# Optimization experiments

Measured on AMD Instinct MI355X. Metric: run time of the kernel, lower is better.

The kernel has to match this reference:

```python
import jax, jax.numpy as jnp
import numpy as np

B, T, L, IN, D, H = 2, 16, 256, 768, 1024, 16
HD = D // H
NREG = 4
P = NREG + 2          # frozen prefix: registers + noise + action
DEPTH = 8
TINT = 4              # temporal_attention_interval
CTX = 30              # temporal_context_length
BASE = 1000.0         # rope_base
EPS = 1e-6            # qk_norm_eps / rmsnorm eps
HID = 4096            # 4.0 * latent_dim
S = L + P             # tokens per frame


def _rms(x, w=None, eps=EPS):
    y = x * jax.lax.rsqrt(jnp.mean(x * x, axis=-1, keepdims=True) + eps)
    return y * w if w is not None else y


def _rope_cache(n, hd, base):
    inv = base ** (-jnp.arange(0, hd, 2, dtype=jnp.float32) / hd)
    ang = jnp.arange(n, dtype=jnp.float32)[:, None] * inv[None, :]  # [n, hd/2]
    return jnp.cos(ang), jnp.sin(ang)


def _apply_rope(x, cos, sin):
    x1, x2 = x[..., ::2], x[..., 1::2]
    return jnp.stack([x1 * cos - x2 * sin, x1 * sin + x2 * cos], axis=-1).reshape(x.shape)


def _attn(x, Wqkv, Wo, cos, sin, mask):
    # x: [..., S, D]; mask: bool, True = attend, broadcastable to [..., H, S, S]
    qkv = x @ Wqkv
    q, k, v = jnp.split(qkv, 3, axis=-1)
    heads = lambda t: t.reshape(t.shape[:-1] + (H, HD)).swapaxes(-2, -3)  # [..., H, S, HD]
    q, k, v = heads(q), heads(k), heads(v)
    q = _apply_rope(_rms(q), cos, sin)   # qk-norm then RoPE
    k = _apply_rope(_rms(k), cos, sin)
    s = jnp.einsum('...qd,...kd->...qk', q, k) / jnp.sqrt(jnp.float32(HD))
    s = jnp.where(mask, s, jnp.float32(-1e9))
    p = jax.nn.softmax(s, axis=-1) * mask.any(axis=-1, keepdims=True)  # zero rows with no allowed keys
    o = jnp.einsum('...qk,...kd->...qd', p, v)
    return o.swapaxes(-2, -3).reshape(x.shape) @ Wo


def _spatial_mask():
    m = np.zeros((S, S), bool)
    r, n, a, ls = NREG, NREG, NREG + 1, NREG + 2
    m[ls:, ls:] = True; m[ls:, n] = True; m[ls:, a] = True; m[ls:, :r] = True
    m[n, n] = True; m[a, a] = True
    m[:r, ls:] = True; m[:r, n] = True; m[:r, a] = True; m[:r, :r] = True
    return jnp.asarray(m)


def _temporal_mask(indep):
    m = jnp.tril(jnp.ones((T, T), bool), -1)  # strictly-past causal
    if CTX is not None and CTX < T:
        m = m & jnp.triu(m, -CTX)             # sliding context window
    m = jnp.broadcast_to(m, (B, T, T))
    m = jnp.where(indep[:, None, None], False, m)
    return m[:, None, None]  # [B,1,1,T,T] -> broadcasts over token pos and heads


def setup_inputs() -> dict:
    key = jax.random.key(0)
    ks = iter(jax.random.split(key, 40))
    g = lambda shape, s=0.02: jax.random.normal(next(ks), shape, jnp.float32) * s
    inp = {
        'noisy_latents': jax.random.normal(next(ks), (B, T, L, IN), jnp.float32),
        'noise_levels': jax.random.uniform(next(ks), (B, T), jnp.float32),
        'actions': jax.random.normal(next(ks), (B, T, 6), jnp.float32),
        'independent_frames_mask': jnp.zeros((B,), bool),
        'actions_mask': jnp.ones((B, T), bool),
        'W_in': g((IN, D)),
        'noise_w1': g((1, D)), 'noise_b1': jnp.zeros((D,), jnp.float32),
        'noise_w2': g((D, D)), 'noise_b2': jnp.zeros((D,), jnp.float32),
        'base_action_embed': g((D,)),
        'action_w': g((6, D)), 'action_b': jnp.zeros((D,), jnp.float32),
        'registers': g((NREG, D)),
        'ln1_w': jnp.ones((DEPTH, D), jnp.float32),
        'Wqkv_s': g((DEPTH, D, 3 * D)), 'Wo_s': g((DEPTH, D, D)),
        'lnt_w': jnp.ones((DEPTH, D), jnp.float32),
        'Wqkv_t': g((DEPTH, D, 3 * D)), 'Wo_t': g((DEPTH, D, D)),
        'ln2_w': jnp.ones((DEPTH, D), jnp.float32),
        'W1': g((DEPTH, D, HID)), 'W2': g((DEPTH, D, HID)), 'W3': g((DEPTH, HID, D)),
        'final_w': jnp.ones((D,), jnp.float32),
        'W_out': g((D, IN)), 'b_out': jnp.zeros((IN,), jnp.float32),
    }
    return inp


def reference(noisy_latents, noise_levels, actions, independent_frames_mask, actions_mask,
              W_in, noise_w1, noise_b1, noise_w2, noise_b2, base_action_embed,
              action_w, action_b, registers, ln1_w, Wqkv_s, Wo_s, lnt_w, Wqkv_t, Wo_t,
              ln2_w, W1, W2, W3, final_w, W_out, b_out):
    noisy_tokens = noisy_latents @ W_in                                   # [B,T,L,D]
    base = jnp.broadcast_to(base_action_embed, (B, T, 1, D))
    act = base + (actions @ action_w + action_b)[:, :, None, :]
    act = jnp.where(actions_mask[:, :, None, None], act, base)            # [B,T,1,D]
    nz = jax.nn.silu(noise_levels[..., None] @ noise_w1 + noise_b1) @ noise_w2 + noise_b2
    nz = nz[:, :, None, :]                                                # [B,T,1,D]
    reg = jnp.broadcast_to(registers, (B, T, NREG, D))
    x = jnp.concatenate([reg, nz, act, noisy_tokens], axis=2)             # [B,T,S,D]

    sp_mask = _spatial_mask()
    tm_mask = _temporal_mask(independent_frames_mask)
    sp_cos, sp_sin = _rope_cache(S, HD, BASE)
    tm_cos, tm_sin = _rope_cache(T, HD, BASE)
    keep_tok = (jnp.arange(S) >= P)[None, :, None, None]                  # zero temporal update on frozen prefix

    for i in range(DEPTH):
        h = _rms(x, ln1_w[i])
        x = x + _attn(h, Wqkv_s[i], Wo_s[i], sp_cos, sp_sin, sp_mask)
        if i % TINT == 0:
            ht = _rms(x, lnt_w[i]).transpose(0, 2, 1, 3)                  # [B,S,T,D]
            ot = _attn(ht, Wqkv_t[i], Wo_t[i], tm_cos, tm_sin, tm_mask)
            x = x + (ot * keep_tok).transpose(0, 2, 1, 3)
        h2 = _rms(x, ln2_w[i])
        x = x + (jax.nn.silu(h2 @ W1[i]) * (h2 @ W2[i])) @ W3[i]

    latents = _rms(x[..., P:, :], final_w)
    pred_clean_latents = latents @ W_out + b_out                          # [B,T,L,IN]
    return pred_clean_latents
```

## Files before the change

kernel.cpp:

```cpp
#include <hip/hip_runtime.h>
#include <cstdint>
#include <cstddef>

#define DEV __device__ __forceinline__

typedef __attribute__((ext_vector_type(8))) __bf16 bf16x8;
typedef __attribute__((ext_vector_type(4))) float f32x4;

#define NTOK   8384
#define NTOKP  8448
#define NLAT   8192

DEV float b2f(unsigned short u) {
  unsigned int x = ((unsigned int)u) << 16;
  return __builtin_bit_cast(float, x);
}
DEV unsigned short f2b(float f) {
  unsigned int x = __builtin_bit_cast(unsigned int, f);
  x += 0x7fffu + ((x >> 16) & 1u);
  return (unsigned short)(x >> 16);
}
DEV float wred_sum(float v) {
#pragma unroll
  for (int o = 32; o; o >>= 1) v += __shfl_xor(v, o);
  return v;
}
DEV bool mask_or(const void* p, int i) {
  return ((const unsigned char*)p)[i] != 0 || ((const int*)p)[i] != 0;
}
DEV bool mask_and(const void* p, int i) {
  return ((const unsigned char*)p)[i] != 0 && ((const int*)p)[i] != 0;
}


__global__ void conv_f2b(const float* __restrict__ in, unsigned short* __restrict__ out, int n4) {
  int i = blockIdx.x * 256 + threadIdx.x;
  if (i < n4) {
    float4 v = ((const float4*)in)[i];
    ushort4 o;
    o.x = f2b(v.x); o.y = f2b(v.y); o.z = f2b(v.z); o.w = f2b(v.w);
    ((ushort4*)out)[i] = o;
  }
}

__global__ void build_rope(float2* __restrict__ out, int npos) {
  int idx = blockIdx.x * 256 + threadIdx.x;
  if (idx >= npos * 32) return;
  int pos = idx >> 5, i = idx & 31;
  float inv = powf(1000.0f, -(float)(2 * i) * (1.0f / 64.0f));
  float ang = (float)pos * inv;
  float sv, cv;
  sincosf(ang, &sv, &cv);
  out[idx] = make_float2(cv, sv);
}

__global__ __launch_bounds__(256) void transpose_w(const float* __restrict__ in,
                                                   unsigned short* __restrict__ out,
                                                   int K, int N, int ostride, int mode) {
  __shared__ float tile[32][33];
  int kb = blockIdx.x * 32, nb = blockIdx.y * 32;
  int tx = threadIdx.x & 31, ty = threadIdx.x >> 5;
#pragma unroll
  for (int i = 0; i < 32; i += 8)
    tile[ty + i][tx] = in[(size_t)(kb + ty + i) * N + (nb + tx)];
  __syncthreads();
#pragma unroll
  for (int i = 0; i < 32; i += 8) {
    int n = nb + ty + i;
    int row = n;
    if (mode == 1) row = ((n >> 4) << 5) | (n & 15);
    else if (mode == 2) row = (((n >> 4) << 5) + 16) | (n & 15);
    out[(size_t)row * ostride + (kb + tx)] = f2b(tile[tx][ty + i]);
  }
}

__global__ __launch_bounds__(256) void noise_h1(const float* __restrict__ nlvl,
                                                const float* __restrict__ w1,
                                                const float* __restrict__ b1,
                                                const float* __restrict__ b2,
                                                float* __restrict__ h1,
                                                float* __restrict__ nz) {
  int i = blockIdx.x * 256 + threadIdx.x;
  int bt = i >> 10, d = i & 1023;
  float v = nlvl[bt] * w1[d] + b1[d];
  h1[i] = v / (1.0f + expf(-v));
  nz[i] = b2[d];
}

__global__ __launch_bounds__(256) void noise_mm(const float* __restrict__ h1,
                                                const float* __restrict__ w2,
                                                float* __restrict__ nz) {
  __shared__ float hs[32][128];
  int kc = blockIdx.x >> 4, dpg = blockIdx.x & 15;
  int tid = threadIdx.x;
  int k0 = kc * 128;
  for (int idx = tid; idx < 32 * 128; idx += 256) {
    int bt = idx >> 7, k = idx & 127;
    hs[bt][k] = h1[bt * 1024 + k0 + k];
  }
  __syncthreads();
  int dp = dpg * 64 + (tid & 63);
  int bt0 = (tid >> 6) * 8;
  float acc[8] = {};
  for (int k = 0; k < 128; ++k) {
    float w = w2[(size_t)(k0 + k) * 1024 + dp];
#pragma unroll
    for (int j = 0; j < 8; ++j) acc[j] += hs[bt0 + j][k] * w;
  }
#pragma unroll
  for (int j = 0; j < 8; ++j) atomicAdd(&nz[(bt0 + j) * 1024 + dp], acc[j]);
}

__global__ void embed_special(float* __restrict__ x, const float* __restrict__ regs,
                              const float* __restrict__ nz, const float* __restrict__ base_emb,
                              const float* __restrict__ actions, const float* __restrict__ action_w,
                              const float* __restrict__ action_b,
                              const void* __restrict__ amask) {
  int bt = blockIdx.x, d = threadIdx.x;
  float* xr = x + (size_t)bt * 262 * 1024;
#pragma unroll
  for (int r = 0; r < 4; ++r) xr[r * 1024 + d] = regs[r * 1024 + d];
  xr[4 * 1024 + d] = nz[(size_t)bt * 1024 + d];
  float a = base_emb[d];
  if (mask_or(amask, bt)) {
    float s = action_b[d];
#pragma unroll
    for (int i = 0; i < 6; ++i) s += actions[bt * 6 + i] * action_w[i * 1024 + d];
    a += s;
  }
  xr[5 * 1024 + d] = a;
}

template <bool REMAP>
__global__ __launch_bounds__(256) void rms_k(const float* __restrict__ x,
                                             const float* __restrict__ w,
                                             unsigned short* __restrict__ out) {
  int m = blockIdx.x, tid = threadIdx.x;
  size_t src = REMAP ? ((size_t)(m >> 8) * 262 + 6 + (m & 255)) : (size_t)m;
  float4 v = ((const float4*)(x + src * 1024))[tid];
  float ss = v.x * v.x + v.y * v.y + v.z * v.z + v.w * v.w;
  ss = wred_sum(ss);
  __shared__ float sred[4];
  if ((tid & 63) == 0) sred[tid >> 6] = ss;
  __syncthreads();
  float tot = sred[0] + sred[1] + sred[2] + sred[3];
  float sc = rsqrtf(tot * (1.0f / 1024.0f) + 1e-6f);
  float4 wv = ((const float4*)w)[tid];
  ushort4 o;
  o.x = f2b(v.x * sc * wv.x); o.y = f2b(v.y * sc * wv.y);
  o.z = f2b(v.z * sc * wv.z); o.w = f2b(v.w * sc * wv.w);
  ((ushort4*)(out + (size_t)m * 1024))[tid] = o;
}

#define KSTR 72
#define VSTR 296
__global__ __launch_bounds__(256) void attn_spatial(const unsigned short* __restrict__ qkv,
                                                    unsigned short* __restrict__ o,
                                                    const float2* __restrict__ rope) {
  __shared__ unsigned short Ks[272 * KSTR];
  __shared__ unsigned short Vt[64 * VSTR];
  __shared__ unsigned short Ps[4][16 * VSTR];
  const int h = blockIdx.x & 15;
  const int bt = blockIdx.x >> 4;
  const int tid = threadIdx.x, wave = tid >> 6, lane = tid & 63;
  const size_t tb = (size_t)bt * 262;

  {
    const int d = lane;
#pragma unroll 1
    for (int pss = 0; pss < 17; ++pss) {
      const int t0 = (pss * 4 + wave) * 4;
      ushort4 vp;
      unsigned short* vpp = (unsigned short*)&vp;
#pragma unroll
      for (int j = 0; j < 4; ++j) {
        const int t = t0 + j;
        float kv = 0.f, vv = 0.f;
        if (t < 262) {
          const size_t rb = (tb + t) * 3072 + h * 64 + d;
          kv = b2f(qkv[rb + 1024]);
          vv = b2f(qkv[rb + 2048]);
        }
        float ss = wred_sum(kv * kv);
        kv *= rsqrtf(ss * (1.0f / 64.0f) + 1e-6f);
        float partner = __shfl_xor(kv, 1);
        const int tc = t < 262 ? t : 261;
        float2 cs = rope[tc * 32 + (d >> 1)];
        kv = ((d & 1) == 0) ? (kv * cs.x - partner * cs.y)
                            : (partner * cs.y + kv * cs.x);
        Ks[t * KSTR + d] = f2b(kv);
        vpp[j] = f2b(vv);
      }
      *(ushort4*)(&Vt[d * VSTR + t0]) = vp;
    }
    for (int idx = tid; idx < 64 * 24; idx += 256) {
      Vt[(idx / 24) * VSTR + 272 + (idx % 24)] = 0;
    }
    for (int idx = tid; idx < 4 * 16 * 34; idx += 256) {
      int w = idx / (16 * 34), r = (idx / 34) & 15, c = idx % 34;
      Ps[w][r * VSTR + 262 + c] = 0;
    }
  }
  __syncthreads();

  unsigned short* Pw = &Ps[wave][0];
  const int kcol = lane & 15;
  const int g8 = (lane >> 4) << 3;
  const int g4 = g8 >> 1;
  const int rq = (lane >> 4) << 2;

#pragma unroll 1
  for (int qc = wave; qc < 17; qc += 4) {
    const int q0 = qc * 16;
    const int qrow = q0 + kcol;
    const int grow = qrow < 262 ? qrow : 261;
    const unsigned short* qp = qkv + (tb + grow) * 3072 + h * 64 + g8;
    float qv[16];
    {
      ushort4 a = *(const ushort4*)qp, b = *(const ushort4*)(qp + 4);
      ushort4 c = *(const ushort4*)(qp + 32), e = *(const ushort4*)(qp + 36);
      qv[0] = b2f(a.x); qv[1] = b2f(a.y); qv[2] = b2f(a.z); qv[3] = b2f(a.w);
      qv[4] = b2f(b.x); qv[5] = b2f(b.y); qv[6] = b2f(b.z); qv[7] = b2f(b.w);
      qv[8] = b2f(c.x); qv[9] = b2f(c.y); qv[10] = b2f(c.z); qv[11] = b2f(c.w);
      qv[12] = b2f(e.x); qv[13] = b2f(e.y); qv[14] = b2f(e.z); qv[15] = b2f(e.w);
    }
    float ss = 0.f;
#pragma unroll
    for (int i = 0; i < 16; ++i) ss += qv[i] * qv[i];
    ss += __shfl_xor(ss, 16);
    ss += __shfl_xor(ss, 32);
    const float qsc = rsqrtf(ss * (1.0f / 64.0f) + 1e-6f);
    bf16x8 aq0, aq1;
    unsigned short* u0 = (unsigned short*)&aq0;
    unsigned short* u1 = (unsigned short*)&aq1;
#pragma unroll
    for (int i = 0; i < 4; ++i) {
      float2 cs0 = rope[grow * 32 + g4 + i];
      float a = qv[2 * i] * qsc, b = qv[2 * i + 1] * qsc;
      u0[2 * i] = f2b(a * cs0.x - b * cs0.y);
      u0[2 * i + 1] = f2b(a * cs0.y + b * cs0.x);
      float2 cs1 = rope[grow * 32 + 16 + g4 + i];
      float a1 = qv[8 + 2 * i] * qsc, b1 = qv[9 + 2 * i] * qsc;
      u1[2 * i] = f2b(a1 * cs1.x - b1 * cs1.y);
      u1[2 * i + 1] = f2b(a1 * cs1.y + b1 * cs1.x);
    }
    f32x4 sc[17];
#pragma unroll
    for (int kc = 0; kc < 17; ++kc) {
      const unsigned short* kb = &Ks[(kc * 16 + kcol) * KSTR + g8];
      f32x4 z = {};
      z = __builtin_amdgcn_mfma_f32_16x16x32_bf16(aq0, *(const bf16x8*)kb, z, 0, 0, 0);
      sc[kc] = __builtin_amdgcn_mfma_f32_16x16x32_bf16(aq1, *(const bf16x8*)(kb + 32), z, 0, 0, 0);
    }
#pragma unroll
    for (int kc = 0; kc < 17; ++kc) {
      const int k = kc * 16 + kcol;
#pragma unroll
      for (int j = 0; j < 4; ++j) {
        const int sq = q0 + rq + j;
        const bool valid = (k < 262) && ((sq != 4 && sq != 5) || (k == sq));
        sc[kc][j] = valid ? sc[kc][j] * 0.125f : -1e30f;
      }
    }
    float sm[4];
#pragma unroll
    for (int j = 0; j < 4; ++j) {
      float m = -1e30f;
#pragma unroll
      for (int kc = 0; kc < 17; ++kc) m = fmaxf(m, sc[kc][j]);
#pragma unroll
      for (int off = 1; off < 16; off <<= 1) m = fmaxf(m, __shfl_xor(m, off));
      float s = 0.f;
#pragma unroll
      for (int kc = 0; kc < 17; ++kc) {
        float e = expf(sc[kc][j] - m);
        sc[kc][j] = e;
        s += e;
      }
#pragma unroll
      for (int off = 1; off < 16; off <<= 1) s += __shfl_xor(s, off);
      sm[j] = 1.0f / s;
    }
#pragma unroll
    for (int kc = 0; kc < 17; ++kc) {
      const int k = kc * 16 + kcol;
#pragma unroll
      for (int j = 0; j < 4; ++j)
        Pw[(rq + j) * VSTR + k] = f2b(sc[kc][j] * sm[j]);
    }
    f32x4 oacc[4] = {};
#pragma unroll
    for (int tc = 0; tc < 9; ++tc) {
      const bf16x8 ap = *(const bf16x8*)(&Pw[kcol * VSTR + tc * 32 + g8]);
#pragma unroll
      for (int nt = 0; nt < 4; ++nt) {
        const bf16x8 bv = *(const bf16x8*)(&Vt[(nt * 16 + kcol) * VSTR + tc * 32 + g8]);
        oacc[nt] = __builtin_amdgcn_mfma_f32_16x16x32_bf16(ap, bv, oacc[nt], 0, 0, 0);
      }
    }
#pragma unroll
    for (int nt = 0; nt < 4; ++nt) {
#pragma unroll
      for (int j = 0; j < 4; ++j) {
        const int sq = q0 + rq + j;
        if (sq < 262)
          o[(tb + sq) * 1024 + h * 64 + nt * 16 + kcol] = f2b(oacc[nt][j]);
      }
    }
  }
}

__global__ __launch_bounds__(256) void attn_temporal(const unsigned short* __restrict__ qkv,
                                                     unsigned short* __restrict__ o,
                                                     const float2* __restrict__ rope,
                                                     const void* __restrict__ indep) {
  int gw = blockIdx.x * 4 + (threadIdx.x >> 6);
  int lane = threadIdx.x & 63;
  if (gw >= NTOK) return;
  int h = gw & 15;
  int s = (gw >> 4) % 262;
  int b = (gw >> 4) / 262;
  bool dead = (s < 6) || mask_and(indep, b);
  float q[16], kk[16], vv[16], out[16];
#pragma unroll
  for (int t = 0; t < 16; ++t) {
    out[t] = 0.f;
    if (!dead) {
      size_t off = ((size_t)((b * 16 + t) * 262 + s)) * 3072 + h * 64 + lane;
      q[t] = b2f(qkv[off]);
      kk[t] = b2f(qkv[off + 1024]);
      vv[t] = b2f(qkv[off + 2048]);
    }
  }
  if (!dead) {
#pragma unroll
    for (int t = 0; t < 16; ++t) {
      float sq_ = wred_sum(q[t] * q[t]);
      float qv = q[t] * rsqrtf(sq_ * (1.0f / 64.0f) + 1e-6f);
      float sk_ = wred_sum(kk[t] * kk[t]);
      float kv = kk[t] * rsqrtf(sk_ * (1.0f / 64.0f) + 1e-6f);
      float2 cs = rope[t * 32 + (lane >> 1)];
      float qp = __shfl_xor(qv, 1);
      float kp = __shfl_xor(kv, 1);
      q[t] = ((lane & 1) == 0) ? (qv * cs.x - qp * cs.y) : (qp * cs.y + qv * cs.x);
      kk[t] = ((lane & 1) == 0) ? (kv * cs.x - kp * cs.y) : (kp * cs.y + kv * cs.x);
    }
#pragma unroll
    for (int t = 1; t < 16; ++t) {
      float m = -1e30f, l = 0.f, acc = 0.f;
#pragma unroll
      for (int j = 0; j < t; ++j) {
        float pr = q[t] * kk[j];
#pragma unroll
        for (int o2 = 32; o2; o2 >>= 1) pr += __shfl_xor(pr, o2);
        pr *= 0.125f;
        float mn = fmaxf(m, pr);
        float cor = expf(m - mn);
        float e = expf(pr - mn);
        l = l * cor + e;
        acc = acc * cor + e * vv[j];
        m = mn;
      }
      out[t] = acc / l;
    }
  }
#pragma unroll
  for (int t = 0; t < 16; ++t) {
    size_t off = ((size_t)((b * 16 + t) * 262 + s)) * 1024 + h * 64 + lane;
    o[off] = f2b(out[t]);
  }
}

DEV void stage_tiles(const unsigned short* __restrict__ A, const unsigned short* __restrict__ Bw,
                     size_t arow0, size_t brow0, int lda, int k0,
                     unsigned short* As, unsigned short* Bs, int wave, int lane) {
  const int srow = lane >> 2;
  const int scol = (lane & 3) * 8;
#pragma unroll
  for (int c = 0; c < 2; ++c) {
    const int chunk = wave * 2 + c;
    unsigned short* ga = const_cast<unsigned short*>(A + (arow0 + chunk * 16 + srow) * lda + k0 + scol);
    unsigned short* gb = const_cast<unsigned short*>(Bw + (brow0 + chunk * 16 + srow) * lda + k0 + scol);
    __builtin_amdgcn_global_load_lds((__attribute__((address_space(1))) void*)ga,
                                     (__attribute__((address_space(3))) void*)(As + chunk * 512),
                                     16, 0, 0);
    __builtin_amdgcn_global_load_lds((__attribute__((address_space(1))) void*)gb,
                                     (__attribute__((address_space(3))) void*)(Bs + chunk * 512),
                                     16, 0, 0);
  }
}

template <int EPI>
__global__ __launch_bounds__(256) void gemm_k(const unsigned short* __restrict__ A,
                                              const unsigned short* __restrict__ Bw,
                                              void* __restrict__ C,
                                              const float* __restrict__ aux,
                                              int Mvalid, int K, int lda, int ldc) {
  __shared__ unsigned short As[2][128 * 32];
  __shared__ unsigned short Bs[2][128 * 32];
  const int tid = threadIdx.x;
  const int wave = tid >> 6, lane = tid & 63;
  const int wm = wave >> 1, wn = wave & 1;
  const size_t arow0 = (size_t)blockIdx.x * 128;
  const size_t brow0 = (size_t)blockIdx.y * 128;

  f32x4 acc[4][4] = {};
  const int KT = K >> 5;

  stage_tiles(A, Bw, arow0, brow0, lda, 0, As[0], Bs[0], wave, lane);
  __syncthreads();
  int buf = 0;
  for (int kt = 0; kt < KT; ++kt) {
    if (kt + 1 < KT)
      stage_tiles(A, Bw, arow0, brow0, lda, (kt + 1) << 5, As[buf ^ 1], Bs[buf ^ 1], wave, lane);
    const int kk = (lane >> 4) * 8;
    const int rsel = lane & 15;
    bf16x8 af[4], bfr[4];
#pragma unroll
    for (int mt = 0; mt < 4; ++mt)
      af[mt] = *reinterpret_cast<const bf16x8*>(&As[buf][(wm * 64 + mt * 16 + rsel) * 32 + kk]);
#pragma unroll
    for (int nt = 0; nt < 4; ++nt)
      bfr[nt] = *reinterpret_cast<const bf16x8*>(&Bs[buf][(wn * 64 + nt * 16 + rsel) * 32 + kk]);
#pragma unroll
    for (int mt = 0; mt < 4; ++mt) {
#pragma unroll
      for (int nt = 0; nt < 4; ++nt)
        acc[mt][nt] = __builtin_amdgcn_mfma_f32_16x16x32_bf16(af[mt], bfr[nt], acc[mt][nt], 0, 0, 0);
    }
    __syncthreads();
    buf ^= 1;
  }

  const int rsel = lane & 15;
  const int row_base = blockIdx.x * 128 + wm * 64;
  const int col_base = blockIdx.y * 128 + wn * 64;

  if (EPI == 2) {
    const int cg0 = blockIdx.y * 64 + wn * 32;
#pragma unroll
    for (int mt = 0; mt < 4; ++mt) {
#pragma unroll
      for (int pr = 0; pr < 2; ++pr) {
        const int col = cg0 + pr * 16 + rsel;
        const int r0 = row_base + mt * 16 + ((lane >> 4) << 2);
#pragma unroll
        for (int j = 0; j < 4; ++j) {
          const int row = r0 + j;
          if (row < Mvalid) {
            float u1 = acc[mt][pr * 2][j];
            float u2 = acc[mt][pr * 2 + 1][j];
            float sv = u1 / (1.0f + expf(-u1));
            ((unsigned short*)C)[(size_t)row * ldc + col] = f2b(sv * u2);
          }
        }
      }
    }
    return;
  }

#pragma unroll
  for (int mt = 0; mt < 4; ++mt) {
#pragma unroll
    for (int nt = 0; nt < 4; ++nt) {
      const int col = col_base + nt * 16 + rsel;
      const int r0 = row_base + mt * 16 + ((lane >> 4) << 2);
#pragma unroll
      for (int j = 0; j < 4; ++j) {
        const int row = r0 + j;
        float v = acc[mt][nt][j];
        if (row < Mvalid) {
          if (EPI == 0) {
            ((unsigned short*)C)[(size_t)row * ldc + col] = f2b(v);
          } else if (EPI == 1) {
            float* p = (float*)C + (size_t)row * ldc + col;
            *p += v;
          } else if (EPI == 3) {
            ((float*)C)[(size_t)row * ldc + col] = v + aux[col];
          } else if (EPI == 5) {
            int xr = (row >> 8) * 262 + 6 + (row & 255);
            ((float*)C)[(size_t)xr * ldc + col] = v;
          }
        }
      }
    }
  }
}

extern "C" void kernel_launch(void* const* d_in, const int* in_sizes, int n_in,
                              void* d_out, int out_size, void* d_ws, size_t ws_size,
                              hipStream_t stream) {
  const float* noisy = (const float*)d_in[0];
  const float* nlvl = (const float*)d_in[1];
  const float* actions = (const float*)d_in[2];
  const void* indep = d_in[3];
  const void* amask = d_in[4];
  const float* W_in = (const float*)d_in[5];
  const float* noise_w1 = (const float*)d_in[6];
  const float* noise_b1 = (const float*)d_in[7];
  const float* noise_w2 = (const float*)d_in[8];
  const float* noise_b2 = (const float*)d_in[9];
  const float* base_emb = (const float*)d_in[10];
  const float* action_w = (const float*)d_in[11];
  const float* action_b = (const float*)d_in[12];
  const float* registers = (const float*)d_in[13];
  const float* ln1_w = (const float*)d_in[14];
  const float* Wqkv_s = (const float*)d_in[15];
  const float* Wo_s = (const float*)d_in[16];
  const float* lnt_w = (const float*)d_in[17];
  const float* Wqkv_t = (const float*)d_in[18];
  const float* Wo_t = (const float*)d_in[19];
  const float* ln2_w = (const float*)d_in[20];
  const float* W1 = (const float*)d_in[21];
  const float* W2 = (const float*)d_in[22];
  const float* W3 = (const float*)d_in[23];
  const float* final_w = (const float*)d_in[24];
  const float* W_out = (const float*)d_in[25];
  const float* b_out = (const float*)d_in[26];

  char* p = (char*)d_ws;
  auto alloc = [&](size_t bytes) {
    char* r = p;
    p += (bytes + 255) & ~(size_t)255;
    return r;
  };
  float* X = (float*)alloc((size_t)NTOKP * 1024 * 4);
  unsigned short* HB = (unsigned short*)alloc((size_t)NTOKP * 1024 * 2);
  unsigned short* AO = (unsigned short*)alloc((size_t)NTOKP * 1024 * 2);
  char* SCR = alloc((size_t)NTOKP * 4096 * 2);
  unsigned short* QKV = (unsigned short*)SCR;
  unsigned short* G = (unsigned short*)SCR;
  unsigned short* NLB = (unsigned short*)SCR;
  float* NZ = (float*)alloc(32 * 1024 * 4);
  float* H1 = (float*)alloc(32 * 1024 * 4);
  float2* RSP = (float2*)alloc(262 * 32 * 8);
  float2* RTM = (float2*)alloc(16 * 32 * 8);
  unsigned short* WINT = (unsigned short*)alloc((size_t)1024 * 768 * 2);
  unsigned short* WQKVS = (unsigned short*)alloc((size_t)8 * 3072 * 1024 * 2);
  unsigned short* WOS = (unsigned short*)alloc((size_t)8 * 1024 * 1024 * 2);
  unsigned short* WQKVT = (unsigned short*)alloc((size_t)2 * 3072 * 1024 * 2);
  unsigned short* WOT = (unsigned short*)alloc((size_t)2 * 1024 * 1024 * 2);
  unsigned short* W12T = (unsigned short*)alloc((size_t)8 * 8192 * 1024 * 2);
  unsigned short* W3T = (unsigned short*)alloc((size_t)8 * 1024 * 4096 * 2);
  unsigned short* WOUTT = (unsigned short*)alloc((size_t)768 * 1024 * 2);

  auto tr = [&](const float* in, unsigned short* out, int K, int N, int ostride, int mode) {
    dim3 g(K / 32, N / 32);
    transpose_w<<<g, 256, 0, stream>>>(in, out, K, N, ostride, mode);
  };
  tr(W_in, WINT, 768, 1024, 768, 0);
  for (int i = 0; i < 8; ++i) {
    tr(Wqkv_s + (size_t)i * 1024 * 3072, WQKVS + (size_t)i * 3072 * 1024, 1024, 3072, 1024, 0);
    tr(Wo_s + (size_t)i * 1024 * 1024, WOS + (size_t)i * 1024 * 1024, 1024, 1024, 1024, 0);
    tr(W1 + (size_t)i * 1024 * 4096, W12T + (size_t)i * 8192 * 1024, 1024, 4096, 1024, 1);
    tr(W2 + (size_t)i * 1024 * 4096, W12T + (size_t)i * 8192 * 1024, 1024, 4096, 1024, 2);
    tr(W3 + (size_t)i * 4096 * 1024, W3T + (size_t)i * 1024 * 4096, 4096, 1024, 4096, 0);
  }
  for (int s = 0; s < 2; ++s) {
    int i = s * 4;
    tr(Wqkv_t + (size_t)i * 1024 * 3072, WQKVT + (size_t)s * 3072 * 1024, 1024, 3072, 1024, 0);
    tr(Wo_t + (size_t)i * 1024 * 1024, WOT + (size_t)s * 1024 * 1024, 1024, 1024, 1024, 0);
  }
  tr(W_out, WOUTT, 1024, 768, 1024, 0);

  build_rope<<<33, 256, 0, stream>>>(RSP, 262);
  build_rope<<<2, 256, 0, stream>>>(RTM, 16);
  conv_f2b<<<6144, 256, 0, stream>>>(noisy, NLB, (NLAT * 768) / 4);
  noise_h1<<<128, 256, 0, stream>>>(nlvl, noise_w1, noise_b1, noise_b2, H1, NZ);
  noise_mm<<<128, 256, 0, stream>>>(H1, noise_w2, NZ);
  embed_special<<<32, 1024, 0, stream>>>(X, registers, NZ, base_emb, actions, action_w, action_b, amask);
  {
    dim3 g(64, 8);
    gemm_k<5><<<g, 256, 0, stream>>>(NLB, WINT, X, nullptr, NLAT, 768, 768, 1024);
  }

  for (int i = 0; i < 8; ++i) {
    rms_k<false><<<NTOK, 256, 0, stream>>>(X, ln1_w + i * 1024, HB);
    {
      dim3 g(66, 24);
      gemm_k<0><<<g, 256, 0, stream>>>(HB, WQKVS + (size_t)i * 3072 * 1024, QKV, nullptr, NTOK, 1024, 1024, 3072);
    }
    attn_spatial<<<512, 256, 0, stream>>>(QKV, AO, RSP);
    {
      dim3 g(66, 8);
      gemm_k<1><<<g, 256, 0, stream>>>(AO, WOS + (size_t)i * 1024 * 1024, X, nullptr, NTOK, 1024, 1024, 1024);
    }
    if ((i & 3) == 0) {
      const int s = i >> 2;
      rms_k<false><<<NTOK, 256, 0, stream>>>(X, lnt_w + i * 1024, HB);
      {
        dim3 g(66, 24);
        gemm_k<0><<<g, 256, 0, stream>>>(HB, WQKVT + (size_t)s * 3072 * 1024, QKV, nullptr, NTOK, 1024, 1024, 3072);
      }
      attn_temporal<<<2096, 256, 0, stream>>>(QKV, AO, RTM, indep);
      {
        dim3 g(66, 8);
        gemm_k<1><<<g, 256, 0, stream>>>(AO, WOT + (size_t)s * 1024 * 1024, X, nullptr, NTOK, 1024, 1024, 1024);
      }
    }
    rms_k<false><<<NTOK, 256, 0, stream>>>(X, ln2_w + i * 1024, HB);
    {
      dim3 g(66, 64);
      gemm_k<2><<<g, 256, 0, stream>>>(HB, W12T + (size_t)i * 8192 * 1024, G, nullptr, NTOK, 1024, 1024, 4096);
    }
    {
      dim3 g(66, 8);
      gemm_k<1><<<g, 256, 0, stream>>>(G, W3T + (size_t)i * 1024 * 4096, X, nullptr, NTOK, 4096, 4096, 1024);
    }
  }

  rms_k<true><<<NLAT, 256, 0, stream>>>(X, final_w, HB);
  {
    dim3 g(64, 6);
    gemm_k<3><<<g, 256, 0, stream>>>(HB, WOUTT, d_out, b_out, NLAT, 1024, 1024, 768);
  }
}
```

Measured before the change: 5.887 ms.

## Add 256x256 eight-wave pipelined GEMM for fused SwiGLU up-projection

Adds a new 512-thread GEMM kernel with 256x256 tiles, direct global-to-LDS loads into an XOR-swizzled shared layout, and an eight-phase schedule that interleaves prefetch of the next K tile with MFMA work, using barriers and raised wave priority. Only the W1/W2 SwiGLU GEMM uses it. The SiLU-times-gate epilogue moves from the old gemm_k into the new kernel. The aim is more data reuse per tile and better overlap of memory traffic with MFMA. In exchange the kernel uses 128 KB of shared memory and many accumulator registers, which lowers occupancy, and the manual waitcnt accounting is fragile.

```diff
diff --git a/kernel.cpp b/kernel.cpp
--- a/kernel.cpp
+++ b/kernel.cpp
@@ -30,6 +30,11 @@
 }
 DEV bool mask_and(const void* p, int i) {
   return ((const unsigned char*)p)[i] != 0 && ((const int*)p)[i] != 0;
+}
+DEV void wgb() {
+  asm volatile("" ::: "memory");
+  __builtin_amdgcn_s_barrier();
+  asm volatile("" ::: "memory");
 }
 
 
@@ -436,29 +441,6 @@
   const int row_base = blockIdx.x * 128 + wm * 64;
   const int col_base = blockIdx.y * 128 + wn * 64;
 
-  if (EPI == 2) {
-    const int cg0 = blockIdx.y * 64 + wn * 32;
-#pragma unroll
-    for (int mt = 0; mt < 4; ++mt) {
-#pragma unroll
-      for (int pr = 0; pr < 2; ++pr) {
-        const int col = cg0 + pr * 16 + rsel;
-        const int r0 = row_base + mt * 16 + ((lane >> 4) << 2);
-#pragma unroll
-        for (int j = 0; j < 4; ++j) {
-          const int row = r0 + j;
-          if (row < Mvalid) {
-            float u1 = acc[mt][pr * 2][j];
-            float u2 = acc[mt][pr * 2 + 1][j];
-            float sv = u1 / (1.0f + expf(-u1));
-            ((unsigned short*)C)[(size_t)row * ldc + col] = f2b(sv * u2);
-          }
-        }
-      }
-    }
-    return;
-  }
-
 #pragma unroll
   for (int mt = 0; mt < 4; ++mt) {
 #pragma unroll
@@ -481,6 +463,151 @@
             int xr = (row >> 8) * 262 + 6 + (row & 255);
             ((float*)C)[(size_t)xr * ldc + col] = v;
           }
+        }
+      }
+    }
+  }
+}
+
+DEV void stage_half(const unsigned short* __restrict__ G, size_t row0, int lda,
+                    int kt, unsigned short* buf, int half, int tid) {
+#pragma unroll
+  for (int i = 0; i < 2; ++i) {
+    const int p = half * 16384 + i * 8192 + tid * 16;
+    const int l = p ^ (((p >> 9) & 1) << 5);
+    const int grow = l >> 7;
+    const int gcol = (l & 127) >> 1;
+    unsigned short* g = const_cast<unsigned short*>(G + (row0 + grow) * (size_t)lda + kt * 64 + gcol);
+    __builtin_amdgcn_global_load_lds((__attribute__((address_space(1))) void*)g,
+                                     (__attribute__((address_space(3))) void*)(buf + (p >> 1)),
+                                     16, 0, 0);
+  }
+}
+DEV bf16x8 rdfrag(const unsigned short* buf, int row, int kbyte) {
+  const int l = row * 128 + kbyte;
+  const int ph = l ^ (((l >> 9) & 1) << 5);
+  return *(const bf16x8*)((const char*)buf + ph);
+}
+
+#define PHASE8(as_, bs_, mtp, LOADB, SLOT, ENDW)                                  \
+  {                                                                               \
+    bf16x8 af[2][2];                                                              \
+    if (LOADB) {                                                                  \
+      _Pragma("unroll") for (int nt = 0; nt < 4; ++nt) {                          \
+        _Pragma("unroll") for (int ks = 0; ks < 2; ++ks)                          \
+          bfr[nt][ks] = rdfrag(bs_, wn * 64 + nt * 16 + rsel, ks * 64 + kb16);    \
+      }                                                                           \
+    }                                                                             \
+    _Pragma("unroll") for (int m = 0; m < 2; ++m) {                               \
+      _Pragma("unroll") for (int ks = 0; ks < 2; ++ks)                            \
+        af[m][ks] = rdfrag(as_, wm * 128 + ((mtp)*2 + m) * 16 + rsel, ks * 64 + kb16); \
+    }                                                                             \
+    SLOT;                                                                         \
+    wgb();                                                                        \
+    asm volatile("s_waitcnt lgkmcnt(0)" ::: "memory");                            \
+    __builtin_amdgcn_sched_barrier(0);                                            \
+    __builtin_amdgcn_s_setprio(1);                                                \
+    _Pragma("unroll") for (int m = 0; m < 2; ++m) {                               \
+      _Pragma("unroll") for (int nt = 0; nt < 4; ++nt) {                          \
+        _Pragma("unroll") for (int ks = 0; ks < 2; ++ks)                          \
+          acc[(mtp)*2 + m][nt] = __builtin_amdgcn_mfma_f32_16x16x32_bf16(         \
+              af[m][ks], bfr[nt][ks], acc[(mtp)*2 + m][nt], 0, 0, 0);             \
+      }                                                                           \
+    }                                                                             \
+    __builtin_amdgcn_s_setprio(0);                                                \
+    ENDW;                                                                         \
+    wgb();                                                                        \
+  }
+
+template <int EPI>
+__global__ __launch_bounds__(512) void gemm8p_k(const unsigned short* __restrict__ A,
+                                                const unsigned short* __restrict__ Bw,
+                                                void* __restrict__ C,
+                                                int Mvalid, int K, int lda, int ldc) {
+  __shared__ unsigned short As[2][16384];
+  __shared__ unsigned short Bs[2][16384];
+  const int tid = threadIdx.x;
+  const int lane = tid & 63, wid = tid >> 6;
+  const int wm = wid >> 2, wn = wid & 3;
+  const int rsel = lane & 15;
+  const int kb16 = (lane >> 4) * 16;
+  const size_t arow0 = (size_t)blockIdx.x * 256;
+  const size_t brow0 = (size_t)blockIdx.y * 256;
+  const int NT = K >> 6;
+  const int NITER = NT >> 1;
+
+  f32x4 acc[8][4] = {};
+
+  stage_half(A, arow0, lda, 0, As[0], 0, tid);
+  stage_half(A, arow0, lda, 0, As[0], 1, tid);
+  stage_half(Bw, brow0, lda, 0, Bs[0], 0, tid);
+  stage_half(Bw, brow0, lda, 0, Bs[0], 1, tid);
+  stage_half(Bw, brow0, lda, 1, Bs[1], 0, tid);
+  stage_half(Bw, brow0, lda, 1, Bs[1], 1, tid);
+  asm volatile("s_waitcnt vmcnt(4)" ::: "memory");
+  wgb();
+
+#pragma unroll 1
+  for (int it = 0; it < NITER; ++it) {
+    const int kt0 = it * 2;
+    const bool pf2 = (kt0 + 2) < NT;
+    const bool pf3 = (kt0 + 3) < NT;
+    bf16x8 bfr[4][2];
+    PHASE8(As[0], Bs[0], 0, true,
+           { stage_half(A, arow0, lda, kt0 + 1, As[1], 0, tid); }, {});
+    PHASE8(As[0], Bs[0], 1, false,
+           { stage_half(A, arow0, lda, kt0 + 1, As[1], 1, tid); }, {});
+    PHASE8(As[0], Bs[0], 2, false,
+           { if (pf2) stage_half(Bw, brow0, lda, kt0 + 2, Bs[0], 0, tid); }, {});
+    PHASE8(As[0], Bs[0], 3, false,
+           { if (pf2) stage_half(Bw, brow0, lda, kt0 + 2, Bs[0], 1, tid); },
+           { if (pf2) { asm volatile("s_waitcnt vmcnt(4)" ::: "memory"); }
+             else     { asm volatile("s_waitcnt vmcnt(0)" ::: "memory"); } });
+    PHASE8(As[1], Bs[1], 0, true,
+           { if (pf2) stage_half(A, arow0, lda, kt0 + 2, As[0], 0, tid); }, {});
+    PHASE8(As[1], Bs[1], 1, false,
+           { if (pf2) stage_half(A, arow0, lda, kt0 + 2, As[0], 1, tid); }, {});
+    PHASE8(As[1], Bs[1], 2, false,
+           { if (pf3) stage_half(Bw, brow0, lda, kt0 + 3, Bs[1], 0, tid); }, {});
+    PHASE8(As[1], Bs[1], 3, false,
+           { if (pf3) stage_half(Bw, brow0, lda, kt0 + 3, Bs[1], 1, tid); },
+           { if (pf3) { asm volatile("s_waitcnt vmcnt(4)" ::: "memory"); } });
+  }
+
+  const int row_base = blockIdx.x * 256 + wm * 128;
+  if (EPI == 2) {
+    const int cg0 = blockIdx.y * 128 + wn * 32;
+#pragma unroll
+    for (int mt = 0; mt < 8; ++mt) {
+      const int r0 = row_base + mt * 16 + ((lane >> 4) << 2);
+#pragma unroll
+      for (int pr = 0; pr < 2; ++pr) {
+        const int col = cg0 + pr * 16 + rsel;
+#pragma unroll
+        for (int j = 0; j < 4; ++j) {
+          const int row = r0 + j;
+          if (row < Mvalid) {
+            float u1 = acc[mt][pr * 2][j];
+            float u2 = acc[mt][pr * 2 + 1][j];
+            float sv = u1 / (1.0f + expf(-u1));
+            ((unsigned short*)C)[(size_t)row * ldc + col] = f2b(sv * u2);
+          }
+        }
+      }
+    }
+  } else {
+    const int col_base = blockIdx.y * 256 + wn * 64;
+#pragma unroll
+    for (int mt = 0; mt < 8; ++mt) {
+#pragma unroll
+      for (int nt = 0; nt < 4; ++nt) {
+        const int col = col_base + nt * 16 + rsel;
+        const int r0 = row_base + mt * 16 + ((lane >> 4) << 2);
+#pragma unroll
+        for (int j = 0; j < 4; ++j) {
+          const int row = r0 + j;
+          if (row < Mvalid)
+            ((unsigned short*)C)[(size_t)row * ldc + col] = f2b(acc[mt][nt][j]);
         }
       }
     }
@@ -600,8 +727,8 @@
     }
     rms_k<false><<<NTOK, 256, 0, stream>>>(X, ln2_w + i * 1024, HB);
     {
-      dim3 g(66, 64);
-      gemm_k<2><<<g, 256, 0, stream>>>(HB, W12T + (size_t)i * 8192 * 1024, G, nullptr, NTOK, 1024, 1024, 4096);
+      dim3 g(33, 32);
+      gemm8p_k<2><<<g, 512, 0, stream>>>(HB, W12T + (size_t)i * 8192 * 1024, G, NTOK, 1024, 1024, 4096);
     }
     {
       dim3 g(66, 8);
```

Measured after the change: 6.011 ms. +2.1%, slower.
